# Kernel optimization log

Measured on AMD Instinct MI355X. Metric: run time of the kernel, lower is better.

Reference implementation:

```python
import jax, jax.numpy as jnp
import numpy as np
import math

B, T, D = 2, 2048, 2048
NH, HD = 16, 128          # n_heads, head_dim (expand_factor=1)
LAMBDA_INIT = 0.8 - 0.6 * math.exp(-0.3 * 0)  # layer_depth=0 -> 0.2
EPS = float(jnp.finfo(jnp.float32).eps)


def rms_norm(x):
    return x * jax.lax.rsqrt(jnp.mean(x * x, axis=-1, keepdims=True) + EPS)


def apply_rotary(x, cos, sin):
    # x: (B,T,H,HD); cos/sin: (1,T,1,HD/2); half-split convention
    d = x.shape[-1] // 2
    x1, x2 = x[..., :d], x[..., d:]
    return jnp.concatenate([x1 * cos + x2 * sin, -x1 * sin + x2 * cos], axis=-1)


def causal_attn(q, k, v, scale):
    # q,k: (B,T,H,HD); v: (B,T,H,Dv) -> (B,T,H,Dv)
    Tq = q.shape[1]
    s = jnp.einsum('bqhd,bkhd->bhqk', q, k) * scale
    mask = jnp.tril(jnp.ones((Tq, Tq), dtype=bool))
    s = jnp.where(mask, s, -1e30)
    p = jax.nn.softmax(s, axis=-1)
    return jnp.einsum('bhqk,bkhd->bqhd', p, v)


def setup_inputs():
    key = jax.random.key(0)
    ks = jax.random.split(key, 8)
    x = jax.random.normal(ks[0], (B, T, D), jnp.float32)
    Wq = jax.random.normal(ks[1], (D, NH * HD), jnp.float32) * 0.02
    Wk = jax.random.normal(ks[2], (D, NH * HD), jnp.float32) * 0.02
    Wv = jax.random.normal(ks[3], (D, NH * HD), jnp.float32) * 0.02
    lambda_q1 = jax.random.normal(ks[4], (HD // 2,), jnp.float32) * 0.1
    lambda_k1 = jax.random.normal(ks[5], (HD // 2,), jnp.float32) * 0.1
    lambda_q2 = jax.random.normal(ks[6], (HD // 2,), jnp.float32) * 0.1
    lambda_k2 = jax.random.normal(ks[7], (HD // 2,), jnp.float32) * 0.1
    softmax_scaler = jnp.ones((1, 1, NH, 1), jnp.float32)
    return {"x": x, "Wq": Wq, "Wk": Wk, "Wv": Wv,
            "lambda_q1": lambda_q1, "lambda_k1": lambda_k1,
            "lambda_q2": lambda_q2, "lambda_k2": lambda_k2,
            "softmax_scaler": softmax_scaler}


def reference(x, Wq, Wk, Wv, lambda_q1, lambda_k1, lambda_q2, lambda_k2, softmax_scaler):
    b, t, _ = x.shape
    q = (x @ Wq).reshape(b, t, NH, HD)
    k = (x @ Wk).reshape(b, t, NH, HD)
    v = (x @ Wv).reshape(b, t, NH // 2, 2 * HD)

    # rotary tables (base 10000, dim=HD)
    inv_freq = 1.0 / (10000.0 ** (jnp.arange(0, HD, 2, dtype=jnp.float32) / HD))
    freqs = jnp.arange(t, dtype=jnp.float32)[:, None] * inv_freq[None, :]
    cos = jnp.cos(freqs)[None, :, None, :]
    sin = jnp.sin(freqs)[None, :, None, :]

    # qk-norm then RoPE
    q = apply_rotary(rms_norm(q), cos, sin)
    k = apply_rotary(rms_norm(k), cos, sin)

    k = k.reshape(b, t, 2, NH // 2, HD)
    k1, k2 = k[:, :, 0], k[:, :, 1]

    # scalable softmax: scale q by s * log(position)
    log_pos = jnp.log(jnp.arange(1, t + 1, dtype=jnp.float32)).reshape(1, t, 1, 1)
    q = softmax_scaler * log_pos * q

    q = q.reshape(b, t, 2, NH // 2, HD)
    q1, q2 = q[:, :, 0], q[:, :, 1]

    scale = 1.0 / math.sqrt(HD)  # flash-attn default: 1/sqrt(q head dim)
    y1 = causal_attn(q1, k1, v, scale)
    y2 = causal_attn(q2, k2, v, scale)

    lambda_1 = jnp.exp(jnp.sum(lambda_q1 * lambda_k1))
    lambda_2 = jnp.exp(jnp.sum(lambda_q2 * lambda_k2))
    lambda_full = lambda_1 - lambda_2 + LAMBDA_INIT

    y = (y1 - lambda_full * y2).reshape(b, t, D)
    return y
```

## Files before the change

kernel.cpp:

```cpp
#include <hip/hip_runtime.h>

typedef unsigned short u16;
typedef _Float16 f16;
typedef __attribute__((ext_vector_type(8))) _Float16 half8;
typedef __attribute__((ext_vector_type(4))) _Float16 half4;
typedef __attribute__((ext_vector_type(4))) float f32x4;

#define B_  2
#define T_  2048
#define D_  2048
#define NH_ 16
#define HD_ 128
#define QBLK 64
#define KBLK 32

#define MFMAH(a,b,c) __builtin_amdgcn_mfma_f32_16x16x32_f16((a),(b),(c),0,0,0)

__device__ __forceinline__ void gll16(void* lds, const void* g) {
  __builtin_amdgcn_global_load_lds(
      (const __attribute__((address_space(1))) unsigned int*)(size_t)(g),
      (__attribute__((address_space(3))) unsigned int*)(unsigned int)(size_t)(lds),
      16, 0, 0);
}

__global__ __launch_bounds__(256)
void cast_x_kernel(const float* __restrict__ X, f16* __restrict__ Xb) {
  size_t i = ((size_t)blockIdx.x * 256 + threadIdx.x) * 4;
  float4 v = *(const float4*)(X + i);
  half4 o;
  o.x = (f16)v.x; o.y = (f16)v.y; o.z = (f16)v.z; o.w = (f16)v.w;
  *(half4*)(Xb + i) = o;
}

__global__ __launch_bounds__(256)
void wt_kernel(const float* __restrict__ Wq, const float* __restrict__ Wk,
               const float* __restrict__ Wv, f16* __restrict__ Wt) {
  __shared__ float tile[32][33];
  const int z = blockIdx.z;
  const float* W = z == 0 ? Wq : (z == 1 ? Wk : Wv);
  f16* O = Wt + (size_t)z * (2048 * 2048);
  int k0 = blockIdx.x * 32, n0 = blockIdx.y * 32;
  int tx = threadIdx.x & 31, ty = threadIdx.x >> 5;
#pragma unroll
  for (int s = 0; s < 4; ++s)
    tile[ty + s * 8][tx] = W[(size_t)(k0 + ty + s * 8) * 2048 + n0 + tx];
  __syncthreads();
#pragma unroll
  for (int s = 0; s < 4; ++s)
    O[(size_t)(n0 + ty + s * 8) * 2048 + k0 + tx] = (f16)tile[tx][ty + s * 8];
}

__global__ void rope_table_kernel(float* __restrict__ cosT, float* __restrict__ sinT) {
  int t = blockIdx.x, d = threadIdx.x;
  float invf = exp2f(-(float)d * (13.287712379549449f / 64.f));
  float fr = (float)t * invf;
  cosT[t * 64 + d] = cosf(fr);
  sinT[t * 64 + d] = sinf(fr);
}

__global__ void lambda_kernel(const float* __restrict__ lq1, const float* __restrict__ lk1,
                              const float* __restrict__ lq2, const float* __restrict__ lk2,
                              float* __restrict__ lam) {
  int l = threadIdx.x;
  float a = lq1[l] * lk1[l];
  float b = lq2[l] * lk2[l];
#pragma unroll
  for (int off = 1; off < 64; off <<= 1) { a += __shfl_xor(a, off); b += __shfl_xor(b, off); }
  if (l == 0) lam[0] = expf(a) - expf(b) + 0.2f;
}

__global__ __launch_bounds__(256)
void gemm_qkv_kernel(const f16* __restrict__ Xb, const f16* __restrict__ Wt,
                     float* __restrict__ Qf, float* __restrict__ Kf,
                     f16* __restrict__ Vg) {
  __shared__ f16 As[128 * 32];
  __shared__ f16 Bs[128 * 32];
  const int bid = blockIdx.x, z = blockIdx.y;
  const int lid = ((bid & 7) << 6) | (bid >> 3);
  const int bn = lid >> 5, bm = lid & 31;
  const f16* Bw = Wt + (size_t)z * (2048 * 2048);
  const int tid = threadIdx.x;
  const int w = tid >> 6, l = tid & 63;
  const int li = l & 15, lg = l >> 4;
  const int wr = w >> 1, wc = w & 1;

  f32x4 acc[4][4] = {};

  const int o0 = (w * 2 + 0) * 1024 + l * 16;
  const int o1 = (w * 2 + 1) * 1024 + l * 16;
  const int rA0 = o0 >> 6, rA1 = o1 >> 6;
  const int cs0 = ((o0 >> 4) & 3) ^ (rA0 & 3);
  const int cs1 = ((o1 >> 4) & 3) ^ (rA1 & 3);
  const f16* srcA0 = Xb + (size_t)(bm * 128 + rA0) * 2048 + cs0 * 8;
  const f16* srcA1 = Xb + (size_t)(bm * 128 + rA1) * 2048 + cs1 * 8;
  const f16* srcB0 = Bw + (size_t)(bn * 128 + rA0) * 2048 + cs0 * 8;
  const f16* srcB1 = Bw + (size_t)(bn * 128 + rA1) * 2048 + cs1 * 8;
  char* dstA0 = (char*)As + (w * 2 + 0) * 1024;
  char* dstA1 = (char*)As + (w * 2 + 1) * 1024;
  char* dstB0 = (char*)Bs + (w * 2 + 0) * 1024;
  char* dstB1 = (char*)Bs + (w * 2 + 1) * 1024;

  for (int kt = 0; kt < 64; ++kt) {
    __syncthreads();
    gll16(dstA0, srcA0 + kt * 32);
    gll16(dstA1, srcA1 + kt * 32);
    gll16(dstB0, srcB0 + kt * 32);
    gll16(dstB1, srcB1 + kt * 32);
    __syncthreads();
    half8 af[4], bfr[4];
#pragma unroll
    for (int mi = 0; mi < 4; ++mi) {
      int row = wr * 64 + mi * 16 + li;
      int ch = lg ^ (row & 3);
      af[mi] = *(const half8*)((const char*)As + row * 64 + ch * 16);
    }
#pragma unroll
    for (int ni = 0; ni < 4; ++ni) {
      int row = wc * 64 + ni * 16 + li;
      int ch = lg ^ (row & 3);
      bfr[ni] = *(const half8*)((const char*)Bs + row * 64 + ch * 16);
    }
#pragma unroll
    for (int mi = 0; mi < 4; ++mi)
#pragma unroll
      for (int ni = 0; ni < 4; ++ni)
        acc[mi][ni] = MFMAH(af[mi], bfr[ni], acc[mi][ni]);
  }
  if (z < 2) {
    float* C = z ? Kf : Qf;
#pragma unroll
    for (int mi = 0; mi < 4; ++mi)
#pragma unroll
      for (int ni = 0; ni < 4; ++ni) {
        int n = bn * 128 + wc * 64 + ni * 16 + li;
#pragma unroll
        for (int r = 0; r < 4; ++r) {
          int m = bm * 128 + wr * 64 + mi * 16 + lg * 4 + r;
          C[(size_t)m * 2048 + n] = acc[mi][ni][r];
        }
      }
  } else {
#pragma unroll
    for (int mi = 0; mi < 4; ++mi)
#pragma unroll
      for (int ni = 0; ni < 4; ++ni) {
        int n = bn * 128 + wc * 64 + ni * 16 + li;
#pragma unroll
        for (int r = 0; r < 4; ++r) {
          int m = bm * 128 + wr * 64 + mi * 16 + lg * 4 + r;
          Vg[(size_t)m * 2048 + n] = (f16)acc[mi][ni][r];
        }
      }
  }
}

__global__ __launch_bounds__(256)
void qk_process_kernel(const float* __restrict__ Qf, const float* __restrict__ Kf,
                       const float* __restrict__ cosT, const float* __restrict__ sinT,
                       const float* __restrict__ scaler,
                       f16* __restrict__ Qp, f16* __restrict__ Kp) {
  const int r = blockIdx.x * 4 + (threadIdx.x >> 6);
  const int l = threadIdx.x & 63;
  const bool isQ = (blockIdx.y == 0);
  const float* src = isQ ? Qf : Kf;
  f16* dst = isQ ? Qp : Kp;
  const int b = r >> 15;
  const int t = (r >> 4) & 2047;
  const int h = r & 15;
  float v1 = src[(size_t)r * 128 + l];
  float v2 = src[(size_t)r * 128 + l + 64];
  float ss = v1 * v1 + v2 * v2;
#pragma unroll
  for (int off = 1; off < 64; off <<= 1) ss += __shfl_xor(ss, off);
  float rr = rsqrtf(ss * (1.f / 128.f) + 1.1920929e-07f);
  float c = cosT[t * 64 + l], s = sinT[t * 64 + l];
  float n1 = v1 * rr, n2 = v2 * rr;
  float o1 = n1 * c + n2 * s;
  float o2 = n2 * c - n1 * s;
  if (isQ) {
    float mlt = scaler[h] * logf((float)(t + 1)) * 0.08838834764831845f;
    o1 *= mlt; o2 *= mlt;
  }
  size_t orow = ((size_t)(b * 16 + h) * 2048 + t) * 128;
  dst[orow + l] = (f16)o1;
  dst[orow + l + 64] = (f16)o2;
}

__global__ __launch_bounds__(256)
void v_transpose_kernel(const f16* __restrict__ Vg, f16* __restrict__ Vt) {
  __shared__ f16 tile[32][34];
  const int bz = blockIdx.z;
  const int b = bz >> 3, hv = bz & 7;
  const int t0 = blockIdx.x * 32, dv0 = blockIdx.y * 32;
  const int tx = threadIdx.x & 31, ty = threadIdx.x >> 5;
#pragma unroll
  for (int s = 0; s < 4; ++s) {
    int t = t0 + ty + s * 8;
    tile[ty + s * 8][tx] = Vg[(size_t)(b * 2048 + t) * 2048 + hv * 256 + dv0 + tx];
  }
  __syncthreads();
#pragma unroll
  for (int s = 0; s < 4; ++s) {
    int dv = dv0 + ty + s * 8;
    Vt[((size_t)bz * 256 + dv) * 2048 + t0 + tx] = tile[tx][ty + s * 8];
  }
}

__global__ __launch_bounds__(256, 2)
void attn_kernel(const f16* __restrict__ Qp, const f16* __restrict__ Kp,
                 const f16* __restrict__ Vt,
                 float* __restrict__ Y1, float* __restrict__ Y2) {
  __shared__ f16 Ks[2][KBLK * 128];
  __shared__ f16 Vs[2][256 * KBLK];
  __shared__ f16 Ps[4][16 * 32];

  const int bid = blockIdx.x;
  const int lid = ((bid & 7) << 6) | (bid >> 3);
  const int pr = lid & 15;
  const int bh = lid >> 4;
  const int b = bh >> 4, h = bh & 15;
  const int grp = h >> 3, hv = h & 7;
  const f16* QhP = Qp + (size_t)bh * (T_ * HD_);
  const f16* KhP = Kp + (size_t)bh * (T_ * HD_);
  const f16* Vh = Vt + (size_t)(b * 8 + hv) * (256 * T_);
  float* Ybase = (grp ? Y2 : Y1) + (size_t)(b * 8 + hv) * T_ * 256;

  const int tid = threadIdx.x;
  const int w = tid >> 6, l = tid & 63;
  const int li = l & 15, lg = l >> 4;

  int kRow[2], kCs[2], vDv[4], vCs[4];
#pragma unroll
  for (int i = 0; i < 2; ++i) {
    int o = (w * 2 + i) * 1024 + l * 16;
    kRow[i] = o >> 8;
    kCs[i] = ((o >> 4) & 15) ^ (kRow[i] & 7);
  }
#pragma unroll
  for (int i = 0; i < 4; ++i) {
    int o = (w * 4 + i) * 1024 + l * 16;
    vDv[i] = o >> 6;
    vCs[i] = ((o >> 4) & 3) ^ ((vDv[i] >> 1) & 3);
  }

#define STAGE(bi, kv0)                                                          \
  do {                                                                          \
    _Pragma("unroll")                                                           \
    for (int i = 0; i < 2; ++i)                                                 \
      gll16((char*)Ks[bi] + (w * 2 + i) * 1024,                                 \
            KhP + (size_t)((kv0) + kRow[i]) * 128 + kCs[i] * 8);                \
    _Pragma("unroll")                                                           \
    for (int i = 0; i < 4; ++i)                                                 \
      gll16((char*)Vs[bi] + (w * 4 + i) * 1024,                                 \
            Vh + (size_t)vDv[i] * T_ + (kv0) + vCs[i] * 8);                     \
  } while (0)

  const float L2E = 1.4426950408889634f;

#pragma unroll 1
  for (int t2 = 0; t2 < 2; ++t2) {
    const int qt = t2 ? pr : 31 - pr;
    const int q0 = qt * QBLK + w * 16;

    STAGE(0, 0);

    half8 qf[4];
    {
      const f16* qrow = QhP + (size_t)(q0 + li) * 128;
#pragma unroll
      for (int kc = 0; kc < 4; ++kc)
        qf[kc] = *(const half8*)(qrow + kc * 32 + lg * 8);
    }
    f32x4 acc[16] = {};
    float m[4], se[4];
#pragma unroll
    for (int r = 0; r < 4; ++r) { m[r] = -1e30f; se[r] = 0.f; }

    const int nkv = (qt + 1) * 2;
    for (int kv = 0; kv < nkv; ++kv) {
      const int kv0 = kv * KBLK;
      const int cur = kv & 1;
      if (kv + 1 < nkv) {
        STAGE(cur ^ 1, kv0 + KBLK);
        asm volatile("s_waitcnt vmcnt(6)" ::: "memory");
      } else {
        asm volatile("s_waitcnt vmcnt(0)" ::: "memory");
      }
      __builtin_amdgcn_s_barrier();
      if (kv0 <= q0 + 15) {
        f32x4 s0 = {}, s1 = {}, s0b = {}, s1b = {};
        __builtin_amdgcn_s_setprio(1);
#pragma unroll
        for (int kc = 0; kc < 2; ++kc) {
          int ch = kc * 4 + lg;
          int off0 = li * 256 + ((ch ^ (li & 7)) * 16);
          int off1 = (li + 16) * 256 + ((ch ^ (li & 7)) * 16);
          const half8 k0 = *(const half8*)((const char*)Ks[cur] + off0);
          const half8 k1 = *(const half8*)((const char*)Ks[cur] + off1);
          s0 = MFMAH(qf[kc], k0, s0);
          s1 = MFMAH(qf[kc], k1, s1);
        }
#pragma unroll
        for (int kc = 2; kc < 4; ++kc) {
          int ch = kc * 4 + lg;
          int off0 = li * 256 + ((ch ^ (li & 7)) * 16);
          int off1 = (li + 16) * 256 + ((ch ^ (li & 7)) * 16);
          const half8 k0 = *(const half8*)((const char*)Ks[cur] + off0);
          const half8 k1 = *(const half8*)((const char*)Ks[cur] + off1);
          s0b = MFMAH(qf[kc], k0, s0b);
          s1b = MFMAH(qf[kc], k1, s1b);
        }
        __builtin_amdgcn_s_setprio(0);
        s0 += s0b; s1 += s1b;

        float v0[4], v1[4], tmx[4];
        const bool nomask = (kv0 + 31 <= q0);
#pragma unroll
        for (int r = 0; r < 4; ++r) {
          float a = s0[r], bb = s1[r];
          if (!nomask) {
            const int qr = q0 + lg * 4 + r;
            if (kv0 + li > qr) a = -1e30f;
            if (kv0 + 16 + li > qr) bb = -1e30f;
          }
          float t = fmaxf(a, bb);
          t = fmaxf(t, __shfl_xor(t, 1));
          t = fmaxf(t, __shfl_xor(t, 2));
          t = fmaxf(t, __shfl_xor(t, 4));
          t = fmaxf(t, __shfl_xor(t, 8));
          v0[r] = a; v1[r] = bb; tmx[r] = t;
        }
        int need = (tmx[0] > m[0] + 8.f) | (tmx[1] > m[1] + 8.f) |
                   (tmx[2] > m[2] + 8.f) | (tmx[3] > m[3] + 8.f);
        if (__any(need)) {
          float corr[4];
#pragma unroll
          for (int r = 0; r < 4; ++r) {
            float mn = fmaxf(m[r], tmx[r]);
            corr[r] = exp2f((m[r] - mn) * L2E);
            m[r] = mn;
            se[r] *= corr[r];
          }
#pragma unroll
          for (int nt = 0; nt < 16; ++nt) {
            f32x4 a = acc[nt];
            a[0] *= corr[0]; a[1] *= corr[1]; a[2] *= corr[2]; a[3] *= corr[3];
            acc[nt] = a;
          }
        }
        f16* Pw = &Ps[w][0];
#pragma unroll
        for (int r = 0; r < 4; ++r) {
          float p0 = exp2f((v0[r] - m[r]) * L2E);
          float p1 = exp2f((v1[r] - m[r]) * L2E);
          float rs = p0 + p1;
          rs += __shfl_xor(rs, 1);
          rs += __shfl_xor(rs, 2);
          rs += __shfl_xor(rs, 4);
          rs += __shfl_xor(rs, 8);
          se[r] += rs;
          const int rowA = lg * 4 + r;
          const int x = (rowA >> 1) & 3;
          Pw[rowA * 32 + (((li >> 3) ^ x) * 8) + (li & 7)] = (f16)p0;
          Pw[rowA * 32 + ((((li >> 3) | 2) ^ x) * 8) + (li & 7)] = (f16)p1;
        }
        const half8 pa = *(const half8*)(Pw + li * 32 + ((lg ^ ((li >> 1) & 3)) * 8));
        __builtin_amdgcn_s_setprio(1);
#pragma unroll
        for (int nt = 0; nt < 16; ++nt) {
          const int dv = nt * 16 + li;
          const int ch = lg ^ ((dv >> 1) & 3);
          const half8 vf = *(const half8*)((const char*)Vs[cur] + dv * 64 + ch * 16);
          acc[nt] = MFMAH(pa, vf, acc[nt]);
        }
        __builtin_amdgcn_s_setprio(0);
      }
      __builtin_amdgcn_s_barrier();
    }
    float inv[4];
#pragma unroll
    for (int r = 0; r < 4; ++r) inv[r] = 1.0f / se[r];
    float* Yout = Ybase + (size_t)(qt * QBLK) * 256;
#pragma unroll
    for (int nt = 0; nt < 16; ++nt)
#pragma unroll
      for (int r = 0; r < 4; ++r)
        Yout[(size_t)(w * 16 + lg * 4 + r) * 256 + nt * 16 + li] = acc[nt][r] * inv[r];
  }
#undef STAGE
}

__global__ __launch_bounds__(256)
void combine_kernel(const float* __restrict__ Y1, const float* __restrict__ Y2,
                    const float* __restrict__ lamp, float* __restrict__ out) {
  size_t f = ((size_t)blockIdx.x * 256 + threadIdx.x) * 4;
  int dv = (int)(f & 255);
  int hv = (int)((f >> 8) & 7);
  size_t bt = f >> 11;
  int t = (int)(bt & 2047);
  int b = (int)(bt >> 11);
  const float lam = lamp[0];
  size_t yi = ((size_t)(b * 8 + hv) * 2048 + t) * 256 + dv;
  float4 a = *(const float4*)(Y1 + yi);
  float4 c = *(const float4*)(Y2 + yi);
  float4 o;
  o.x = a.x - lam * c.x; o.y = a.y - lam * c.y;
  o.z = a.z - lam * c.z; o.w = a.w - lam * c.w;
  *(float4*)(out + f) = o;
}

extern "C" void kernel_launch(void* const* d_in, const int* in_sizes, int n_in,
                              void* d_out, int out_size, void* d_ws, size_t ws_size,
                              hipStream_t stream) {
  const float* x   = (const float*)d_in[0];
  const float* Wq  = (const float*)d_in[1];
  const float* Wk  = (const float*)d_in[2];
  const float* Wv  = (const float*)d_in[3];
  const float* lq1 = (const float*)d_in[4];
  const float* lk1 = (const float*)d_in[5];
  const float* lq2 = (const float*)d_in[6];
  const float* lk2 = (const float*)d_in[7];
  const float* scl = (const float*)d_in[8];
  float* out = (float*)d_out;

  char* ws = (char*)d_ws;
  f16*  Xb  = (f16*)(ws + 0);
  f16*  Wt  = (f16*)(ws + 16777216);
  float* Qf = (float*)(ws + 41943040);
  float* Kf = (float*)(ws + 75497472);
  f16*  Vg  = (f16*)(ws + 109051904);
  f16*  Vt  = (f16*)(ws + 125829120);
  float* cosT = (float*)(ws + 142606336);
  float* sinT = (float*)(ws + 143130624);
  float* lam  = (float*)(ws + 143654912);
  f16*  Qp = (f16*)(ws + 0);
  f16*  Kp = (f16*)(ws + 16777216);
  float* Y1 = (float*)(ws + 41943040);
  float* Y2 = (float*)(ws + 75497472);

  cast_x_kernel<<<8192, 256, 0, stream>>>(x, Xb);
  wt_kernel<<<dim3(64, 64, 3), 256, 0, stream>>>(Wq, Wk, Wv, Wt);
  rope_table_kernel<<<2048, 64, 0, stream>>>(cosT, sinT);
  lambda_kernel<<<1, 64, 0, stream>>>(lq1, lk1, lq2, lk2, lam);
  gemm_qkv_kernel<<<dim3(512, 3), 256, 0, stream>>>(Xb, Wt, Qf, Kf, Vg);
  qk_process_kernel<<<dim3(16384, 2), 256, 0, stream>>>(Qf, Kf, cosT, sinT, scl, Qp, Kp);
  v_transpose_kernel<<<dim3(64, 8, 16), 256, 0, stream>>>(Vg, Vt);
  attn_kernel<<<512, 256, 0, stream>>>(Qp, Kp, Vt, Y1, Y2);
  combine_kernel<<<8192, 256, 0, stream>>>(Y1, Y2, lam, out);
}
```

Measured before the change: 377.4 us.

## Fuse qk-norm/RoPE into QKV GEMM epilogue, double-buffer GEMM, fp16 attention outputs

The qk_process kernel is folded into the QKV GEMM epilogue. RMS norm is reduced across lanes and waves through shared memory, and RoPE is applied on interleaved columns, which the weight transpose produces by permuting Q/K output rows. The GEMM main loop is double-buffered with async global-to-LDS loads, and the separate fp32 Q/K intermediates are removed. Attention outputs Y1/Y2 are stored as fp16 and combined with vectorized loads, and the cast kernel handles 8 elements per thread. Together these cut intermediate memory traffic and a kernel launch, at the cost of extra precision loss in the fp16 outputs and more epilogue work in the GEMM.

```diff
diff --git a/kernel.cpp b/kernel.cpp
--- a/kernel.cpp
+++ b/kernel.cpp
@@ -25,11 +25,13 @@
 
 __global__ __launch_bounds__(256)
 void cast_x_kernel(const float* __restrict__ X, f16* __restrict__ Xb) {
-  size_t i = ((size_t)blockIdx.x * 256 + threadIdx.x) * 4;
-  float4 v = *(const float4*)(X + i);
-  half4 o;
-  o.x = (f16)v.x; o.y = (f16)v.y; o.z = (f16)v.z; o.w = (f16)v.w;
-  *(half4*)(Xb + i) = o;
+  size_t i = ((size_t)blockIdx.x * 256 + threadIdx.x) * 8;
+  float4 v0 = *(const float4*)(X + i);
+  float4 v1 = *(const float4*)(X + i + 4);
+  half8 o;
+  o[0] = (f16)v0.x; o[1] = (f16)v0.y; o[2] = (f16)v0.z; o[3] = (f16)v0.w;
+  o[4] = (f16)v1.x; o[5] = (f16)v1.y; o[6] = (f16)v1.z; o[7] = (f16)v1.w;
+  *(half8*)(Xb + i) = o;
 }
 
 __global__ __launch_bounds__(256)
@@ -46,8 +48,15 @@
     tile[ty + s * 8][tx] = W[(size_t)(k0 + ty + s * 8) * 2048 + n0 + tx];
   __syncthreads();
 #pragma unroll
-  for (int s = 0; s < 4; ++s)
-    O[(size_t)(n0 + ty + s * 8) * 2048 + k0 + tx] = (f16)tile[tx][ty + s * 8];
+  for (int s = 0; s < 4; ++s) {
+    int nrow = n0 + ty + s * 8;
+    int orow = nrow;
+    if (z < 2) {
+      int hh = nrow >> 7, dd = nrow & 127;
+      orow = (hh << 7) | ((dd & 63) << 1) | (dd >> 6);
+    }
+    O[(size_t)orow * 2048 + k0 + tx] = (f16)tile[tx][ty + s * 8];
+  }
 }
 
 __global__ void rope_table_kernel(float* __restrict__ cosT, float* __restrict__ sinT) {
@@ -71,10 +80,13 @@
 
 __global__ __launch_bounds__(256)
 void gemm_qkv_kernel(const f16* __restrict__ Xb, const f16* __restrict__ Wt,
-                     float* __restrict__ Qf, float* __restrict__ Kf,
+                     const float* __restrict__ cosT, const float* __restrict__ sinT,
+                     const float* __restrict__ scaler,
+                     f16* __restrict__ Qp, f16* __restrict__ Kp,
                      f16* __restrict__ Vg) {
-  __shared__ f16 As[128 * 32];
-  __shared__ f16 Bs[128 * 32];
+  __shared__ f16 As[2][128 * 32];
+  __shared__ f16 Bs[2][128 * 32];
+  __shared__ float ps[4][64];
   const int bid = blockIdx.x, z = blockIdx.y;
   const int lid = ((bid & 7) << 6) | (bid >> 3);
   const int bn = lid >> 5, bm = lid & 31;
@@ -95,51 +107,51 @@
   const f16* srcA1 = Xb + (size_t)(bm * 128 + rA1) * 2048 + cs1 * 8;
   const f16* srcB0 = Bw + (size_t)(bn * 128 + rA0) * 2048 + cs0 * 8;
   const f16* srcB1 = Bw + (size_t)(bn * 128 + rA1) * 2048 + cs1 * 8;
-  char* dstA0 = (char*)As + (w * 2 + 0) * 1024;
-  char* dstA1 = (char*)As + (w * 2 + 1) * 1024;
-  char* dstB0 = (char*)Bs + (w * 2 + 0) * 1024;
-  char* dstB1 = (char*)Bs + (w * 2 + 1) * 1024;
-
+  const int c0 = (w * 2 + 0) * 1024, c1 = (w * 2 + 1) * 1024;
+
+#define GSTAGE(bi, kt)                                         \
+  do {                                                         \
+    gll16((char*)As[bi] + c0, srcA0 + (kt) * 32);              \
+    gll16((char*)As[bi] + c1, srcA1 + (kt) * 32);              \
+    gll16((char*)Bs[bi] + c0, srcB0 + (kt) * 32);              \
+    gll16((char*)Bs[bi] + c1, srcB1 + (kt) * 32);              \
+  } while (0)
+
+  GSTAGE(0, 0);
   for (int kt = 0; kt < 64; ++kt) {
-    __syncthreads();
-    gll16(dstA0, srcA0 + kt * 32);
-    gll16(dstA1, srcA1 + kt * 32);
-    gll16(dstB0, srcB0 + kt * 32);
-    gll16(dstB1, srcB1 + kt * 32);
-    __syncthreads();
+    const int cur = kt & 1;
+    if (kt < 63) {
+      GSTAGE(cur ^ 1, kt + 1);
+      asm volatile("s_waitcnt vmcnt(4)" ::: "memory");
+    } else {
+      asm volatile("s_waitcnt vmcnt(0)" ::: "memory");
+    }
+    __builtin_amdgcn_s_barrier();
     half8 af[4], bfr[4];
 #pragma unroll
     for (int mi = 0; mi < 4; ++mi) {
       int row = wr * 64 + mi * 16 + li;
       int ch = lg ^ (row & 3);
-      af[mi] = *(const half8*)((const char*)As + row * 64 + ch * 16);
+      af[mi] = *(const half8*)((const char*)As[cur] + row * 64 + ch * 16);
     }
 #pragma unroll
     for (int ni = 0; ni < 4; ++ni) {
       int row = wc * 64 + ni * 16 + li;
       int ch = lg ^ (row & 3);
-      bfr[ni] = *(const half8*)((const char*)Bs + row * 64 + ch * 16);
-    }
+      bfr[ni] = *(const half8*)((const char*)Bs[cur] + row * 64 + ch * 16);
+    }
+    __builtin_amdgcn_s_setprio(1);
 #pragma unroll
     for (int mi = 0; mi < 4; ++mi)
 #pragma unroll
       for (int ni = 0; ni < 4; ++ni)
         acc[mi][ni] = MFMAH(af[mi], bfr[ni], acc[mi][ni]);
-  }
-  if (z < 2) {
-    float* C = z ? Kf : Qf;
-#pragma unroll
-    for (int mi = 0; mi < 4; ++mi)
-#pragma unroll
-      for (int ni = 0; ni < 4; ++ni) {
-        int n = bn * 128 + wc * 64 + ni * 16 + li;
-#pragma unroll
-        for (int r = 0; r < 4; ++r) {
-          int m = bm * 128 + wr * 64 + mi * 16 + lg * 4 + r;
-          C[(size_t)m * 2048 + n] = acc[mi][ni][r];
-        }
-      }
-  } else {
+    __builtin_amdgcn_s_setprio(0);
+    __builtin_amdgcn_s_barrier();
+  }
+#undef GSTAGE
+
+  if (z == 2) {
 #pragma unroll
     for (int mi = 0; mi < 4; ++mi)
 #pragma unroll
@@ -151,39 +163,58 @@
           Vg[(size_t)m * 2048 + n] = (f16)acc[mi][ni][r];
         }
       }
-  }
-}
-
-__global__ __launch_bounds__(256)
-void qk_process_kernel(const float* __restrict__ Qf, const float* __restrict__ Kf,
-                       const float* __restrict__ cosT, const float* __restrict__ sinT,
-                       const float* __restrict__ scaler,
-                       f16* __restrict__ Qp, f16* __restrict__ Kp) {
-  const int r = blockIdx.x * 4 + (threadIdx.x >> 6);
-  const int l = threadIdx.x & 63;
-  const bool isQ = (blockIdx.y == 0);
-  const float* src = isQ ? Qf : Kf;
-  f16* dst = isQ ? Qp : Kp;
-  const int b = r >> 15;
-  const int t = (r >> 4) & 2047;
-  const int h = r & 15;
-  float v1 = src[(size_t)r * 128 + l];
-  float v2 = src[(size_t)r * 128 + l + 64];
-  float ss = v1 * v1 + v2 * v2;
-#pragma unroll
-  for (int off = 1; off < 64; off <<= 1) ss += __shfl_xor(ss, off);
-  float rr = rsqrtf(ss * (1.f / 128.f) + 1.1920929e-07f);
-  float c = cosT[t * 64 + l], s = sinT[t * 64 + l];
-  float n1 = v1 * rr, n2 = v2 * rr;
-  float o1 = n1 * c + n2 * s;
-  float o2 = n2 * c - n1 * s;
-  if (isQ) {
-    float mlt = scaler[h] * logf((float)(t + 1)) * 0.08838834764831845f;
-    o1 *= mlt; o2 *= mlt;
-  }
-  size_t orow = ((size_t)(b * 16 + h) * 2048 + t) * 128;
-  dst[orow + l] = (f16)o1;
-  dst[orow + l + 64] = (f16)o2;
+    return;
+  }
+
+  float ss[4][4];
+#pragma unroll
+  for (int mi = 0; mi < 4; ++mi)
+#pragma unroll
+    for (int r = 0; r < 4; ++r) {
+      float s = acc[mi][0][r] * acc[mi][0][r] + acc[mi][1][r] * acc[mi][1][r] +
+                acc[mi][2][r] * acc[mi][2][r] + acc[mi][3][r] * acc[mi][3][r];
+      s += __shfl_xor(s, 1);
+      s += __shfl_xor(s, 2);
+      s += __shfl_xor(s, 4);
+      s += __shfl_xor(s, 8);
+      ss[mi][r] = s;
+    }
+  if (li == 0) {
+#pragma unroll
+    for (int mi = 0; mi < 4; ++mi)
+#pragma unroll
+      for (int r = 0; r < 4; ++r)
+        ps[w][mi * 16 + lg * 4 + r] = ss[mi][r];
+  }
+  __syncthreads();
+
+  const int h = bn;
+  f16* dst = z ? Kp : Qp;
+  const float sch = scaler[h] * 0.08838834764831845f;
+#pragma unroll
+  for (int mi = 0; mi < 4; ++mi) {
+#pragma unroll
+    for (int r = 0; r < 4; ++r) {
+      const int m = bm * 128 + wr * 64 + mi * 16 + lg * 4 + r;
+      const int t = m & 2047, b = m >> 11;
+      const int idx = mi * 16 + lg * 4 + r;
+      const float tot = ps[wr * 2][idx] + ps[wr * 2 + 1][idx];
+      const float rr = rsqrtf(tot * (1.f / 128.f) + 1.1920929e-07f);
+      const float lm = z ? 1.f : sch * logf((float)(t + 1));
+      f16* drow = dst + ((size_t)(b * 16 + h) * 2048 + t) * 128;
+#pragma unroll
+      for (int ni = 0; ni < 4; ++ni) {
+        const int n = wc * 64 + ni * 16 + li;
+        const int d1 = n >> 1;
+        const float c = cosT[t * 64 + d1], s = sinT[t * 64 + d1];
+        float v = acc[mi][ni][r] * rr;
+        float vp = __shfl_xor(v, 1);
+        float o = (li & 1) ? (v * c - vp * s) : (v * c + vp * s);
+        o *= lm;
+        drow[d1 + (li & 1) * 64] = (f16)o;
+      }
+    }
+  }
 }
 
 __global__ __launch_bounds__(256)
@@ -209,7 +240,7 @@
 __global__ __launch_bounds__(256, 2)
 void attn_kernel(const f16* __restrict__ Qp, const f16* __restrict__ Kp,
                  const f16* __restrict__ Vt,
-                 float* __restrict__ Y1, float* __restrict__ Y2) {
+                 f16* __restrict__ Y1, f16* __restrict__ Y2) {
   __shared__ f16 Ks[2][KBLK * 128];
   __shared__ f16 Vs[2][256 * KBLK];
   __shared__ f16 Ps[4][16 * 32];
@@ -223,7 +254,7 @@
   const f16* QhP = Qp + (size_t)bh * (T_ * HD_);
   const f16* KhP = Kp + (size_t)bh * (T_ * HD_);
   const f16* Vh = Vt + (size_t)(b * 8 + hv) * (256 * T_);
-  float* Ybase = (grp ? Y2 : Y1) + (size_t)(b * 8 + hv) * T_ * 256;
+  f16* Ybase = (grp ? Y2 : Y1) + (size_t)(b * 8 + hv) * T_ * 256;
 
   const int tid = threadIdx.x;
   const int w = tid >> 6, l = tid & 63;
@@ -380,20 +411,21 @@
     float inv[4];
 #pragma unroll
     for (int r = 0; r < 4; ++r) inv[r] = 1.0f / se[r];
-    float* Yout = Ybase + (size_t)(qt * QBLK) * 256;
+    f16* Yout = Ybase + (size_t)(qt * QBLK) * 256;
 #pragma unroll
     for (int nt = 0; nt < 16; ++nt)
 #pragma unroll
       for (int r = 0; r < 4; ++r)
-        Yout[(size_t)(w * 16 + lg * 4 + r) * 256 + nt * 16 + li] = acc[nt][r] * inv[r];
+        Yout[(size_t)(w * 16 + lg * 4 + r) * 256 + nt * 16 + li] =
+            (f16)(acc[nt][r] * inv[r]);
   }
 #undef STAGE
 }
 
 __global__ __launch_bounds__(256)
-void combine_kernel(const float* __restrict__ Y1, const float* __restrict__ Y2,
+void combine_kernel(const f16* __restrict__ Y1, const f16* __restrict__ Y2,
                     const float* __restrict__ lamp, float* __restrict__ out) {
-  size_t f = ((size_t)blockIdx.x * 256 + threadIdx.x) * 4;
+  size_t f = ((size_t)blockIdx.x * 256 + threadIdx.x) * 8;
   int dv = (int)(f & 255);
   int hv = (int)((f >> 8) & 7);
   size_t bt = f >> 11;
@@ -401,12 +433,19 @@
   int b = (int)(bt >> 11);
   const float lam = lamp[0];
   size_t yi = ((size_t)(b * 8 + hv) * 2048 + t) * 256 + dv;
-  float4 a = *(const float4*)(Y1 + yi);
-  float4 c = *(const float4*)(Y2 + yi);
-  float4 o;
-  o.x = a.x - lam * c.x; o.y = a.y - lam * c.y;
-  o.z = a.z - lam * c.z; o.w = a.w - lam * c.w;
-  *(float4*)(out + f) = o;
+  half8 a = *(const half8*)(Y1 + yi);
+  half8 c = *(const half8*)(Y2 + yi);
+  float4 o0, o1;
+  o0.x = (float)a[0] - lam * (float)c[0];
+  o0.y = (float)a[1] - lam * (float)c[1];
+  o0.z = (float)a[2] - lam * (float)c[2];
+  o0.w = (float)a[3] - lam * (float)c[3];
+  o1.x = (float)a[4] - lam * (float)c[4];
+  o1.y = (float)a[5] - lam * (float)c[5];
+  o1.z = (float)a[6] - lam * (float)c[6];
+  o1.w = (float)a[7] - lam * (float)c[7];
+  *(float4*)(out + f) = o0;
+  *(float4*)(out + f + 4) = o1;
 }
 
 extern "C" void kernel_launch(void* const* d_in, const int* in_sizes, int n_in,
@@ -426,25 +465,22 @@
   char* ws = (char*)d_ws;
   f16*  Xb  = (f16*)(ws + 0);
   f16*  Wt  = (f16*)(ws + 16777216);
-  float* Qf = (float*)(ws + 41943040);
-  float* Kf = (float*)(ws + 75497472);
-  f16*  Vg  = (f16*)(ws + 109051904);
-  f16*  Vt  = (f16*)(ws + 125829120);
+  f16*  Qp  = (f16*)(ws + 41943040);
+  f16*  Kp  = (f16*)(ws + 58720256);
+  f16*  Vg  = (f16*)(ws + 75497472);
+  f16*  Vt  = (f16*)(ws + 92274688);
+  f16*  Y1  = (f16*)(ws + 109051904);
+  f16*  Y2  = (f16*)(ws + 125829120);
   float* cosT = (float*)(ws + 142606336);
   float* sinT = (float*)(ws + 143130624);
   float* lam  = (float*)(ws + 143654912);
-  f16*  Qp = (f16*)(ws + 0);
-  f16*  Kp = (f16*)(ws + 16777216);
-  float* Y1 = (float*)(ws + 41943040);
-  float* Y2 = (float*)(ws + 75497472);
-
-  cast_x_kernel<<<8192, 256, 0, stream>>>(x, Xb);
+
+  cast_x_kernel<<<4096, 256, 0, stream>>>(x, Xb);
   wt_kernel<<<dim3(64, 64, 3), 256, 0, stream>>>(Wq, Wk, Wv, Wt);
   rope_table_kernel<<<2048, 64, 0, stream>>>(cosT, sinT);
   lambda_kernel<<<1, 64, 0, stream>>>(lq1, lk1, lq2, lk2, lam);
-  gemm_qkv_kernel<<<dim3(512, 3), 256, 0, stream>>>(Xb, Wt, Qf, Kf, Vg);
-  qk_process_kernel<<<dim3(16384, 2), 256, 0, stream>>>(Qf, Kf, cosT, sinT, scl, Qp, Kp);
+  gemm_qkv_kernel<<<dim3(512, 3), 256, 0, stream>>>(Xb, Wt, cosT, sinT, scl, Qp, Kp, Vg);
   v_transpose_kernel<<<dim3(64, 8, 16), 256, 0, stream>>>(Vg, Vt);
   attn_kernel<<<512, 256, 0, stream>>>(Qp, Kp, Vt, Y1, Y2);
-  combine_kernel<<<8192, 256, 0, stream>>>(Y1, Y2, lam, out);
-}
+  combine_kernel<<<4096, 256, 0, stream>>>(Y1, Y2, lam, out);
+}
```

After: 347.1 us. -8.0%, faster.
